# Performance work log

Hardware: AMD Instinct MI355X
Metric: run time of the kernel (lower is better)

The kernel has to match this reference:

```python
import jax, jax.numpy as jnp
import numpy as np

LAMBDA = 1.0          # lambda_param
SIGMA = 1.0           # RBF bandwidth (sigkernel convention: exp(-||x-y||^2 / sigma))
DYADIC_ORDER = 2
F = 2 ** DYADIC_ORDER # dyadic refinement factor per time axis

B, M_POP, DIM, SEQ_LEN = 4, 16, 8, 65


def _rbf_gram(X, Y):
    # X: (m, L, d), Y: (n, L, d) -> static kernel Gram (m, n, L, L)
    sx = jnp.sum(X * X, -1)                       # (m, L)
    sy = jnp.sum(Y * Y, -1)                       # (n, L)
    inner = jnp.einsum('isd,jtd->ijst', X, Y)     # (m, n, L, L)
    d2 = sx[:, None, :, None] + sy[None, :, None, :] - 2.0 * inner
    return jnp.exp(-d2 / SIGMA)


def _increments(G):
    # double increment of the static Gram over time, then dyadic refinement
    inc = G[..., 1:, 1:] + G[..., :-1, :-1] - G[..., 1:, :-1] - G[..., :-1, 1:]
    inc = jnp.repeat(jnp.repeat(inc, F, axis=-2), F, axis=-1) / (F * F)
    return inc  # (..., S, S) with S = F*(L-1)


def _solve_pde(M):
    # Goursat PDE explicit finite-difference scheme (as in sigkernel):
    # K[i+1,j+1] = (K[i+1,j]+K[i,j+1])*(1 + m/2 + m^2/12) - K[i,j]*(1 - m^2/12)
    dtype = M.dtype
    S = M.shape[0]

    def row_step(prev_row, m_row):
        def cell(k_left, inp):
            k00, k01, m = inp
            a = 1.0 + 0.5 * m + m * m * (1.0 / 12.0)
            b = 1.0 - m * m * (1.0 / 12.0)
            k_new = (k_left + k01) * a - k00 * b
            return k_new, k_new
        _, tail = jax.lax.scan(cell, jnp.asarray(1.0, dtype),
                               (prev_row[:-1], prev_row[1:], m_row))
        new_row = jnp.concatenate([jnp.ones((1,), dtype), tail])
        return new_row, None

    row0 = jnp.ones((S + 1,), dtype)
    last_row, _ = jax.lax.scan(row_step, row0, M)
    return last_row[-1]


def _gram_sig(X, Y):
    # signature kernel Gram matrix: X (m,L,d), Y (n,L,d) -> (m,n)
    Minc = _increments(_rbf_gram(X, Y))
    return jax.vmap(jax.vmap(_solve_pde))(Minc)


def setup_inputs() -> dict:
    key = jax.random.key(0)
    k1, k2 = jax.random.split(key)
    generated_samples = jax.random.normal(k1, (B, M_POP, DIM, SEQ_LEN), dtype=jnp.float32)
    real_sample = jax.random.normal(k2, (B, DIM, SEQ_LEN), dtype=jnp.float32)
    return {"generated_samples": generated_samples, "real_sample": real_sample}


def reference(generated_samples, real_sample):
    # generated_samples: (B, m, dim, L); real_sample: (B, dim, L)
    gen = jnp.swapaxes(generated_samples, -1, -2)          # (B, m, L, d)
    real = jnp.swapaxes(real_sample, -1, -2)[:, None]      # (B, 1, L, d)
    m = gen.shape[1]
    K_XX = jax.vmap(_gram_sig)(gen, gen)                   # (B, m, m)
    K_XY = jax.vmap(_gram_sig)(gen, real)                  # (B, m, 1)
    self_sim = (jnp.sum(K_XX, axis=(-1, -2))
                - jnp.trace(K_XX, axis1=-2, axis2=-1)) / (m * (m - 1))
    cross_sim = jnp.mean(K_XY, axis=(-1, -2))
    return jnp.mean(LAMBDA / 2.0 * self_sim - cross_sim)
```

## Files before the change

### kernel.cpp

```cpp
#include <hip/hip_runtime.h>


#define SEQ   65
#define DIMS  8
#define MPOP  16
#define NBATCH 4
#define NPAIR_XX 120
#define NPAIRS (NBATCH*(NPAIR_XX + MPOP))
#define MST 66

typedef float v2f __attribute__((ext_vector_type(2)));
static __device__ __forceinline__ v2f mk2(float x, float y) { return (v2f){x, y}; }

__device__ __forceinline__ float wave_shr1(float x) {
    int xi = __builtin_bit_cast(int, x);
    int r  = __builtin_amdgcn_update_dpp(xi, xi, 0x138, 0xF, 0xF, false);
    return __builtin_bit_cast(float, r);
}
__device__ __forceinline__ float wave_shl1(float x) {
    int xi = __builtin_bit_cast(int, x);
    int r  = __builtin_amdgcn_update_dpp(xi, xi, 0x130, 0xF, 0xF, false);
    return __builtin_bit_cast(float, r);
}
__device__ __forceinline__ float ldm(const float* base, int idx) {
    return base[idx < 0 ? 0 : idx];
}

struct PS { float l0,l1,l2,l3,b0,b1,b2,b3,cn; };

__device__ __forceinline__ void pde_step(PS& s, float m, bool lane0) {
    float t0 = wave_shr1(s.b0);  t0 = lane0 ? 1.f : t0;
    float t1 = wave_shr1(s.b1);  t1 = lane0 ? 1.f : t1;
    float t2 = wave_shr1(s.b2);  t2 = lane0 ? 1.f : t2;
    float t3 = wave_shr1(s.b3);  t3 = lane0 ? 1.f : t3;
    float c = s.cn; s.cn = t3;
    float mm  = m * m;
    float q12 = mm * (1.0f / 12.0f);
    float a   = (1.0f + q12) + 0.5f * m;
    float nb  = q12 - 1.0f;
    v2f av = mk2(a, a), nv = mk2(nb, nb);
    v2f u01 = av * mk2(t0, t1) + nv * mk2(c,  t0);
    v2f u23 = av * mk2(t2, t3) + nv * mk2(t1, t2);
    float q1 = a * s.l0 + u01.x;
    float q2 = a * q1   + u01.y;
    float q3 = a * q2   + u23.x;
    float q4 = a * q3   + u23.y;
    u01 = av * mk2(q1, q2) + nv * mk2(s.l0, q1);
    u23 = av * mk2(q3, q4) + nv * mk2(q2,  q3);
    float r1 = a * s.l1 + u01.x;
    float r2 = a * r1   + u01.y;
    float r3 = a * r2   + u23.x;
    float r4 = a * r3   + u23.y;
    u01 = av * mk2(r1, r2) + nv * mk2(s.l1, r1);
    u23 = av * mk2(r3, r4) + nv * mk2(r2,  r3);
    float w1 = a * s.l2 + u01.x;
    float w2 = a * w1   + u01.y;
    float w3 = a * w2   + u23.x;
    float w4 = a * w3   + u23.y;
    u01 = av * mk2(w1, w2) + nv * mk2(s.l2, w1);
    u23 = av * mk2(w3, w4) + nv * mk2(w2,  w3);
    float v1 = a * s.l3 + u01.x;
    float v2 = a * v1   + u01.y;
    float v3 = a * v2   + u23.x;
    float v4 = a * v3   + u23.y;
    s.b0=v1; s.b1=v2; s.b2=v3; s.b3=v4;
    s.l0=q4; s.l1=r4; s.l2=w4; s.l3=v4;
}

__global__ __launch_bounds__(64, 1) void sigker_kernel(
    const float* __restrict__ gen,
    const float* __restrict__ realp,
    float* __restrict__ ws,
    unsigned* __restrict__ cnt,
    float* __restrict__ out)
{
    __shared__ __align__(16) float YsF[SEQ * DIMS];
    __shared__ float YnL[SEQ];
    __shared__ float R64[SEQ];
    __shared__ float MmL[64 * MST];

    const int tid = threadIdx.x;
    const int I   = tid;
    const bool lane0 = (I == 0);
    const int bid = blockIdx.x;

    int b, ii, jj; bool cross;
    if (bid < NBATCH * NPAIR_XX) {
        b = bid / NPAIR_XX;
        int p = bid % NPAIR_XX;
        int i = 0, acc = 0;
        while (p >= acc + (MPOP - 1 - i)) { acc += (MPOP - 1 - i); ++i; }
        ii = i; jj = i + 1 + (p - acc); cross = false;
    } else {
        int t = bid - NBATCH * NPAIR_XX;
        b = t / MPOP; ii = t % MPOP; jj = 0; cross = true;
    }

    const float* Xg = gen + (size_t)(b * MPOP + ii) * (DIMS * SEQ);
    const float* Yg = cross ? (realp + (size_t)b * (DIMS * SEQ))
                            : (gen + (size_t)(b * MPOP + jj) * (DIMS * SEQ));

    MmL[MST * I] = 0.f;  MmL[MST * I + 65] = 0.f;
    for (int f = tid; f < SEQ * DIMS; f += 64) {
        int d = f / SEQ, s = f - d * SEQ;
        YsF[s * DIMS + d] = Yg[f];
    }
    v2f x01, x23, x45, x67, z01, z23, z45, z67;
    {
        float xv[DIMS], zv[DIMS];
        #pragma unroll
        for (int d = 0; d < DIMS; ++d) {
            xv[d] = Xg[d * SEQ + I];
            zv[d] = Xg[d * SEQ + 64];
        }
        x01 = mk2(xv[0],xv[1]); x23 = mk2(xv[2],xv[3]);
        x45 = mk2(xv[4],xv[5]); x67 = mk2(xv[6],xv[7]);
        z01 = mk2(zv[0],zv[1]); z23 = mk2(zv[2],zv[3]);
        z45 = mk2(zv[4],zv[5]); z67 = mk2(zv[6],zv[7]);
    }
    float xn0, xn64;
    {
        v2f sx = x01*x01 + x23*x23 + x45*x45 + x67*x67;
        v2f sz = z01*z01 + z23*z23 + z45*z45 + z67*z67;
        xn0 = sx.x + sx.y;  xn64 = sz.x + sz.y;
    }
    __syncthreads();

    for (int t = tid; t < SEQ; t += 64) {
        const float4* yv = (const float4*)&YsF[t * DIMS];
        float4 ya = yv[0], yb = yv[1];
        v2f y01 = mk2(ya.x,ya.y), y23 = mk2(ya.z,ya.w);
        v2f y45 = mk2(yb.x,yb.y), y67 = mk2(yb.z,yb.w);
        v2f sn = y01*y01 + y23*y23 + y45*y45 + y67*y67;
        v2f sd = z01*y01 + z23*y23 + z45*y45 + z67*y67;
        float yn  = sn.x + sn.y;
        float dot = sd.x + sd.y;
        YnL[t] = yn;
        R64[t] = __expf(2.f*dot - xn64 - yn);
    }
    __syncthreads();

    float* mrow = &MmL[MST * I];
    float ep, enp;
    {
        const float4* yv = (const float4*)&YsF[0];
        float4 ya = yv[0], yb = yv[1];
        v2f sd = x01*mk2(ya.x,ya.y) + x23*mk2(ya.z,ya.w)
               + x45*mk2(yb.x,yb.y) + x67*mk2(yb.z,yb.w);
        float e  = __expf(2.f*(sd.x + sd.y) - xn0 - YnL[0]);
        float en = wave_shl1(e);
        en = (I == 63) ? R64[0] : en;
        ep = e; enp = en;
    }
    #pragma unroll 4
    for (int t = 1; t < SEQ; ++t) {
        const float4* yv = (const float4*)&YsF[t * DIMS];
        float4 ya = yv[0], yb = yv[1];
        v2f sd = x01*mk2(ya.x,ya.y) + x23*mk2(ya.z,ya.w)
               + x45*mk2(yb.x,yb.y) + x67*mk2(yb.z,yb.w);
        float e  = __expf(2.f*(sd.x + sd.y) - xn0 - YnL[t]);
        float en = wave_shl1(e);
        en = (I == 63) ? R64[t] : en;
        mrow[t] = ((en - enp) + (ep - e)) * (1.0f / 16.0f);
        ep = e; enp = en;
    }

    PS S = {1,1,1,1, 1,1,1,1, 1};
    const int ib = 1 - I;
    float m[8];
    #pragma unroll
    for (int k = 0; k < 8; ++k) m[k] = ldm(mrow, ib + k);

    for (int g = 0; g < 14; ++g) {
        float n[8];
        const int D8 = g * 8 + 8;
        #pragma unroll
        for (int k = 0; k < 8; ++k) n[k] = ldm(mrow, ib + D8 + k);
        #pragma unroll
        for (int k = 0; k < 8; ++k) pde_step(S, m[k], lane0);
        #pragma unroll
        for (int k = 0; k < 8; ++k) m[k] = n[k];
    }
    float mt[7];
    #pragma unroll
    for (int k = 0; k < 7; ++k) mt[k] = ldm(mrow, ib + 120 + k);
    #pragma unroll
    for (int k = 0; k < 8; ++k) pde_step(S, m[k], lane0);
    #pragma unroll
    for (int k = 0; k < 7; ++k) pde_step(S, mt[k], lane0);

    if (tid == 63) {
        float w = cross ? (-1.0f / 32.0f) : (1.0f / 480.0f);
        ws[bid] = w * S.b3;
    }

    __threadfence();
    unsigned old = 0;
    if (tid == 0) old = atomicAdd(cnt, 1u);
    old = __shfl(old, 0);
    if (old == NPAIRS - 1) {
        __threadfence();
        float s = 0.f;
        for (int k = tid; k < NPAIRS; k += 64) s += ws[k];
        #pragma unroll
        for (int off = 32; off >= 1; off >>= 1) s += __shfl_xor(s, off);
        if (tid == 0) out[0] = s;
    }
}

extern "C" void kernel_launch(void* const* d_in, const int* in_sizes, int n_in,
                              void* d_out, int out_size, void* d_ws, size_t ws_size,
                              hipStream_t stream) {
    const float* gen   = (const float*)d_in[0];
    const float* realp = (const float*)d_in[1];
    if (n_in >= 2 && in_sizes[0] == NBATCH * DIMS * SEQ) {
        gen   = (const float*)d_in[1];
        realp = (const float*)d_in[0];
    }
    float*    ws  = (float*)d_ws;
    unsigned* cnt = (unsigned*)((char*)d_ws + NPAIRS * sizeof(float));
    float*    out = (float*)d_out;
    hipMemsetAsync(cnt, 0, sizeof(unsigned), stream);
    sigker_kernel<<<NPAIRS, 64, 0, stream>>>(gen, realp, ws, cnt, out);
}
```

Measured before the change: 91.72 us.

## Split final reduction into second kernel and fold lane0 boundary into DPP old value

```diff
diff --git a/kernel.cpp b/kernel.cpp
--- a/kernel.cpp
+++ b/kernel.cpp
@@ -9,12 +9,9 @@
 #define NPAIRS (NBATCH*(NPAIR_XX + MPOP))
 #define MST 66
 
-typedef float v2f __attribute__((ext_vector_type(2)));
-static __device__ __forceinline__ v2f mk2(float x, float y) { return (v2f){x, y}; }
-
-__device__ __forceinline__ float wave_shr1(float x) {
+__device__ __forceinline__ float wave_shr1_one(float x) {
     int xi = __builtin_bit_cast(int, x);
-    int r  = __builtin_amdgcn_update_dpp(xi, xi, 0x138, 0xF, 0xF, false);
+    int r  = __builtin_amdgcn_update_dpp(0x3f800000, xi, 0x138, 0xF, 0xF, false);
     return __builtin_bit_cast(float, r);
 }
 __device__ __forceinline__ float wave_shl1(float x) {
@@ -28,41 +25,38 @@
 
 struct PS { float l0,l1,l2,l3,b0,b1,b2,b3,cn; };
 
-__device__ __forceinline__ void pde_step(PS& s, float m, bool lane0) {
-    float t0 = wave_shr1(s.b0);  t0 = lane0 ? 1.f : t0;
-    float t1 = wave_shr1(s.b1);  t1 = lane0 ? 1.f : t1;
-    float t2 = wave_shr1(s.b2);  t2 = lane0 ? 1.f : t2;
-    float t3 = wave_shr1(s.b3);  t3 = lane0 ? 1.f : t3;
+__device__ __forceinline__ void pde_step(PS& s, float m) {
+    float t0 = wave_shr1_one(s.b0);
+    float t1 = wave_shr1_one(s.b1);
+    float t2 = wave_shr1_one(s.b2);
+    float t3 = wave_shr1_one(s.b3);
     float c = s.cn; s.cn = t3;
-    float mm  = m * m;
-    float q12 = mm * (1.0f / 12.0f);
+    float q12 = m * m * (1.0f / 12.0f);
     float a   = (1.0f + q12) + 0.5f * m;
     float nb  = q12 - 1.0f;
-    v2f av = mk2(a, a), nv = mk2(nb, nb);
-    v2f u01 = av * mk2(t0, t1) + nv * mk2(c,  t0);
-    v2f u23 = av * mk2(t2, t3) + nv * mk2(t1, t2);
-    float q1 = a * s.l0 + u01.x;
-    float q2 = a * q1   + u01.y;
-    float q3 = a * q2   + u23.x;
-    float q4 = a * q3   + u23.y;
-    u01 = av * mk2(q1, q2) + nv * mk2(s.l0, q1);
-    u23 = av * mk2(q3, q4) + nv * mk2(q2,  q3);
-    float r1 = a * s.l1 + u01.x;
-    float r2 = a * r1   + u01.y;
-    float r3 = a * r2   + u23.x;
-    float r4 = a * r3   + u23.y;
-    u01 = av * mk2(r1, r2) + nv * mk2(s.l1, r1);
-    u23 = av * mk2(r3, r4) + nv * mk2(r2,  r3);
-    float w1 = a * s.l2 + u01.x;
-    float w2 = a * w1   + u01.y;
-    float w3 = a * w2   + u23.x;
-    float w4 = a * w3   + u23.y;
-    u01 = av * mk2(w1, w2) + nv * mk2(s.l2, w1);
-    u23 = av * mk2(w3, w4) + nv * mk2(w2,  w3);
-    float v1 = a * s.l3 + u01.x;
-    float v2 = a * v1   + u01.y;
-    float v3 = a * v2   + u23.x;
-    float v4 = a * v3   + u23.y;
+    float u0 = a*t0 + nb*c;
+    float u1 = a*t1 + nb*t0;
+    float u2 = a*t2 + nb*t1;
+    float u3 = a*t3 + nb*t2;
+    float q1 = a*s.l0 + u0;
+    float q2 = a*q1 + u1;
+    float q3 = a*q2 + u2;
+    float q4 = a*q3 + u3;
+    u0 = a*q1 + nb*s.l0; u1 = a*q2 + nb*q1; u2 = a*q3 + nb*q2; u3 = a*q4 + nb*q3;
+    float r1 = a*s.l1 + u0;
+    float r2 = a*r1 + u1;
+    float r3 = a*r2 + u2;
+    float r4 = a*r3 + u3;
+    u0 = a*r1 + nb*s.l1; u1 = a*r2 + nb*r1; u2 = a*r3 + nb*r2; u3 = a*r4 + nb*r3;
+    float w1 = a*s.l2 + u0;
+    float w2 = a*w1 + u1;
+    float w3 = a*w2 + u2;
+    float w4 = a*w3 + u3;
+    u0 = a*w1 + nb*s.l2; u1 = a*w2 + nb*w1; u2 = a*w3 + nb*w2; u3 = a*w4 + nb*w3;
+    float v1 = a*s.l3 + u0;
+    float v2 = a*v1 + u1;
+    float v3 = a*v2 + u2;
+    float v4 = a*v3 + u3;
     s.b0=v1; s.b1=v2; s.b2=v3; s.b3=v4;
     s.l0=q4; s.l1=r4; s.l2=w4; s.l3=v4;
 }
@@ -70,9 +64,7 @@
 __global__ __launch_bounds__(64, 1) void sigker_kernel(
     const float* __restrict__ gen,
     const float* __restrict__ realp,
-    float* __restrict__ ws,
-    unsigned* __restrict__ cnt,
-    float* __restrict__ out)
+    float* __restrict__ ws)
 {
     __shared__ __align__(16) float YsF[SEQ * DIMS];
     __shared__ float YnL[SEQ];
@@ -81,7 +73,6 @@
 
     const int tid = threadIdx.x;
     const int I   = tid;
-    const bool lane0 = (I == 0);
     const int bid = blockIdx.x;
 
     int b, ii, jj; bool cross;
@@ -105,36 +96,22 @@
         int d = f / SEQ, s = f - d * SEQ;
         YsF[s * DIMS + d] = Yg[f];
     }
-    v2f x01, x23, x45, x67, z01, z23, z45, z67;
-    {
-        float xv[DIMS], zv[DIMS];
-        #pragma unroll
-        for (int d = 0; d < DIMS; ++d) {
-            xv[d] = Xg[d * SEQ + I];
-            zv[d] = Xg[d * SEQ + 64];
-        }
-        x01 = mk2(xv[0],xv[1]); x23 = mk2(xv[2],xv[3]);
-        x45 = mk2(xv[4],xv[5]); x67 = mk2(xv[6],xv[7]);
-        z01 = mk2(zv[0],zv[1]); z23 = mk2(zv[2],zv[3]);
-        z45 = mk2(zv[4],zv[5]); z67 = mk2(zv[6],zv[7]);
-    }
-    float xn0, xn64;
-    {
-        v2f sx = x01*x01 + x23*x23 + x45*x45 + x67*x67;
-        v2f sz = z01*z01 + z23*z23 + z45*z45 + z67*z67;
-        xn0 = sx.x + sx.y;  xn64 = sz.x + sz.y;
+    float x0[DIMS], x64[DIMS];
+    float xn0 = 0.f, xn64 = 0.f;
+    #pragma unroll
+    for (int d = 0; d < DIMS; ++d) {
+        x0[d]  = Xg[d * SEQ + I];   xn0  += x0[d]  * x0[d];
+        x64[d] = Xg[d * SEQ + 64];  xn64 += x64[d] * x64[d];
     }
     __syncthreads();
 
     for (int t = tid; t < SEQ; t += 64) {
         const float4* yv = (const float4*)&YsF[t * DIMS];
         float4 ya = yv[0], yb = yv[1];
-        v2f y01 = mk2(ya.x,ya.y), y23 = mk2(ya.z,ya.w);
-        v2f y45 = mk2(yb.x,yb.y), y67 = mk2(yb.z,yb.w);
-        v2f sn = y01*y01 + y23*y23 + y45*y45 + y67*y67;
-        v2f sd = z01*y01 + z23*y23 + z45*y45 + z67*y67;
-        float yn  = sn.x + sn.y;
-        float dot = sd.x + sd.y;
+        float yn  = ya.x*ya.x + ya.y*ya.y + ya.z*ya.z + ya.w*ya.w
+                  + yb.x*yb.x + yb.y*yb.y + yb.z*yb.z + yb.w*yb.w;
+        float dot = x64[0]*ya.x + x64[1]*ya.y + x64[2]*ya.z + x64[3]*ya.w
+                  + x64[4]*yb.x + x64[5]*yb.y + x64[6]*yb.z + x64[7]*yb.w;
         YnL[t] = yn;
         R64[t] = __expf(2.f*dot - xn64 - yn);
     }
@@ -145,9 +122,9 @@
     {
         const float4* yv = (const float4*)&YsF[0];
         float4 ya = yv[0], yb = yv[1];
-        v2f sd = x01*mk2(ya.x,ya.y) + x23*mk2(ya.z,ya.w)
-               + x45*mk2(yb.x,yb.y) + x67*mk2(yb.z,yb.w);
-        float e  = __expf(2.f*(sd.x + sd.y) - xn0 - YnL[0]);
+        float dot = x0[0]*ya.x + x0[1]*ya.y + x0[2]*ya.z + x0[3]*ya.w
+                  + x0[4]*yb.x + x0[5]*yb.y + x0[6]*yb.z + x0[7]*yb.w;
+        float e  = __expf(2.f*dot - xn0 - YnL[0]);
         float en = wave_shl1(e);
         en = (I == 63) ? R64[0] : en;
         ep = e; enp = en;
@@ -156,9 +133,9 @@
     for (int t = 1; t < SEQ; ++t) {
         const float4* yv = (const float4*)&YsF[t * DIMS];
         float4 ya = yv[0], yb = yv[1];
-        v2f sd = x01*mk2(ya.x,ya.y) + x23*mk2(ya.z,ya.w)
-               + x45*mk2(yb.x,yb.y) + x67*mk2(yb.z,yb.w);
-        float e  = __expf(2.f*(sd.x + sd.y) - xn0 - YnL[t]);
+        float dot = x0[0]*ya.x + x0[1]*ya.y + x0[2]*ya.z + x0[3]*ya.w
+                  + x0[4]*yb.x + x0[5]*yb.y + x0[6]*yb.z + x0[7]*yb.w;
+        float e  = __expf(2.f*dot - xn0 - YnL[t]);
         float en = wave_shl1(e);
         en = (I == 63) ? R64[t] : en;
         mrow[t] = ((en - enp) + (ep - e)) * (1.0f / 16.0f);
@@ -177,7 +154,7 @@
         #pragma unroll
         for (int k = 0; k < 8; ++k) n[k] = ldm(mrow, ib + D8 + k);
         #pragma unroll
-        for (int k = 0; k < 8; ++k) pde_step(S, m[k], lane0);
+        for (int k = 0; k < 8; ++k) pde_step(S, m[k]);
         #pragma unroll
         for (int k = 0; k < 8; ++k) m[k] = n[k];
     }
@@ -185,27 +162,25 @@
     #pragma unroll
     for (int k = 0; k < 7; ++k) mt[k] = ldm(mrow, ib + 120 + k);
     #pragma unroll
-    for (int k = 0; k < 8; ++k) pde_step(S, m[k], lane0);
+    for (int k = 0; k < 8; ++k) pde_step(S, m[k]);
     #pragma unroll
-    for (int k = 0; k < 7; ++k) pde_step(S, mt[k], lane0);
+    for (int k = 0; k < 7; ++k) pde_step(S, mt[k]);
 
     if (tid == 63) {
         float w = cross ? (-1.0f / 32.0f) : (1.0f / 480.0f);
         ws[bid] = w * S.b3;
     }
+}
 
-    __threadfence();
-    unsigned old = 0;
-    if (tid == 0) old = atomicAdd(cnt, 1u);
-    old = __shfl(old, 0);
-    if (old == NPAIRS - 1) {
-        __threadfence();
-        float s = 0.f;
-        for (int k = tid; k < NPAIRS; k += 64) s += ws[k];
-        #pragma unroll
-        for (int off = 32; off >= 1; off >>= 1) s += __shfl_xor(s, off);
-        if (tid == 0) out[0] = s;
-    }
+__global__ __launch_bounds__(64, 1) void sigker_reduce(
+    const float* __restrict__ ws, float* __restrict__ out)
+{
+    const int lane = threadIdx.x;
+    float s = 0.f;
+    for (int k = lane; k < NPAIRS; k += 64) s += ws[k];
+    #pragma unroll
+    for (int off = 32; off >= 1; off >>= 1) s += __shfl_xor(s, off);
+    if (lane == 0) out[0] = s;
 }
 
 extern "C" void kernel_launch(void* const* d_in, const int* in_sizes, int n_in,
@@ -217,9 +192,8 @@
         gen   = (const float*)d_in[1];
         realp = (const float*)d_in[0];
     }
-    float*    ws  = (float*)d_ws;
-    unsigned* cnt = (unsigned*)((char*)d_ws + NPAIRS * sizeof(float));
-    float*    out = (float*)d_out;
-    hipMemsetAsync(cnt, 0, sizeof(unsigned), stream);
-    sigker_kernel<<<NPAIRS, 64, 0, stream>>>(gen, realp, ws, cnt, out);
+    float* ws  = (float*)d_ws;
+    float* out = (float*)d_out;
+    sigker_kernel<<<NPAIRS, 64, 0, stream>>>(gen, realp, ws);
+    sigker_reduce<<<1, 64, 0, stream>>>(ws, out);
 }
```

After: 85.67 us. -6.6%, faster.
